# Optimization experiments

Measured on AMD Instinct MI355X. Metric: run time of the kernel, lower is better.

## Reference

```python
import jax, jax.numpy as jnp
import numpy as np

B, GH, GW, DIM, NH = 1, 48, 64, 1536, 16
HD = DIM // NH          # 96
C = HD // 2             # 48, divisible by 3 as the rope split requires
L = max(GH, GW)


def setup_inputs() -> dict:
    key = jax.random.key(0)
    ks = jax.random.split(key, 6)
    x = jax.random.normal(ks[0], (B, GH * GW, DIM), jnp.float32)
    w_init = lambda k: jax.random.normal(k, (DIM, DIM), jnp.float32) * 0.02
    # rope frequency table: theta[p, j] = p / 10000^(j/C); freqs = exp(i*theta)
    pos = jnp.arange(L, dtype=jnp.float32)[:, None]
    inv = 10000.0 ** (-jnp.arange(C, dtype=jnp.float32) / C)
    theta = pos * inv[None, :]
    return {
        "x": x,
        "wq": w_init(ks[1]), "bq": jnp.zeros((DIM,), jnp.float32),
        "wk": w_init(ks[2]), "bk": jnp.zeros((DIM,), jnp.float32),
        "wv": w_init(ks[3]), "bv": jnp.zeros((DIM,), jnp.float32),
        "wo": w_init(ks[4]), "bo": jnp.zeros((DIM,), jnp.float32),
        "freqs_cos": jnp.cos(theta), "freqs_sin": jnp.sin(theta),
        "h": GH, "w": GW,
    }


def rope_apply_spatial(x, freqs_cos, freqs_sin, h, w):
    # x: [b, s, n, d] with s == h*w. Complex rotation done in real arithmetic.
    b, s, n, d = x.shape
    c = d // 2
    c3 = c // 3
    # channel groups: [0:c3] identity (ones), [c3:2c3] rotated by h-position,
    # [2c3:3c3] rotated by w-position  (matches freqs.split + cat in torch)
    cos_hw = jnp.concatenate([
        jnp.ones((h, w, c3), x.dtype),
        jnp.broadcast_to(freqs_cos[:h, None, c3:2 * c3], (h, w, c3)),
        jnp.broadcast_to(freqs_cos[None, :w, 2 * c3:3 * c3], (h, w, c3)),
    ], axis=-1).reshape(1, s, 1, c)
    sin_hw = jnp.concatenate([
        jnp.zeros((h, w, c3), x.dtype),
        jnp.broadcast_to(freqs_sin[:h, None, c3:2 * c3], (h, w, c3)),
        jnp.broadcast_to(freqs_sin[None, :w, 2 * c3:3 * c3], (h, w, c3)),
    ], axis=-1).reshape(1, s, 1, c)
    xc = x.reshape(b, s, n, c, 2)
    xr, xi = xc[..., 0], xc[..., 1]
    yr = xr * cos_hw - xi * sin_hw
    yi = xr * sin_hw + xi * cos_hw
    return jnp.stack([yr, yi], axis=-1).reshape(b, s, n, d)


def reference(x, wq, bq, wk, bk, wv, bv, wo, bo, freqs_cos, freqs_sin, h, w):
    b, s, _ = x.shape
    q = (x @ wq + bq).reshape(b, s, NH, HD)
    k = (x @ wk + bk).reshape(b, s, NH, HD)
    v = (x @ wv + bv).reshape(b, s, NH, HD)
    q = rope_apply_spatial(q, freqs_cos, freqs_sin, h, w)
    k = rope_apply_spatial(k, freqs_cos, freqs_sin, h, w)
    scale = 1.0 / jnp.sqrt(jnp.asarray(HD, q.dtype))
    scores = jnp.einsum('bqnd,bknd->bnqk', q, k) * scale  # [b, n, s, s]
    attn = jax.nn.softmax(scores, axis=-1)
    out = jnp.einsum('bnqk,bknd->bqnd', attn, v).reshape(b, s, NH * HD)
    return out @ wo + bo
```

## Files before the change

### kernel.cpp

```cpp
#include <hip/hip_runtime.h>
#include <math.h>

#define S_LEN 3072
#define DIM 1536
#define NHEADS 16
#define HDIM 96
#define NPAIR 48

typedef __attribute__((ext_vector_type(8))) _Float16 half8;
typedef __attribute__((ext_vector_type(4))) _Float16 half4v;
typedef __attribute__((ext_vector_type(2))) _Float16 half2v;
typedef __attribute__((ext_vector_type(4))) float f32x4;

__device__ inline void gload16(const void* g, void* l) {
    __builtin_amdgcn_global_load_lds(
        (const __attribute__((address_space(1))) void*)g,
        (__attribute__((address_space(3))) void*)l, 16, 0, 0);
}

__device__ inline unsigned int packh2(float a, float b) {
    _Float16 ha = (_Float16)a, hb = (_Float16)b;
    unsigned short ua = *(unsigned short*)&ha;
    unsigned short ub = *(unsigned short*)&hb;
    return (unsigned int)ua | ((unsigned int)ub << 16);
}

__global__ __launch_bounds__(256)
void convert_f32_f16(const float* __restrict__ src, _Float16* __restrict__ dst, int n4)
{
    int i = blockIdx.x * 256 + threadIdx.x;
    if (i < n4) {
        float4 v = *(const float4*)&src[(size_t)i * 4];
        half4v h = { (_Float16)v.x, (_Float16)v.y, (_Float16)v.z, (_Float16)v.w };
        *(half4v*)&dst[(size_t)i * 4] = h;
    }
}

__global__ __launch_bounds__(256)
void transpose_w(const float* __restrict__ w0, const float* __restrict__ w1,
                 const float* __restrict__ w2, const float* __restrict__ w3,
                 _Float16* __restrict__ wt)
{
    __shared__ _Float16 t[64][68];
    const int z = blockIdx.z;
    const float* W = (z == 0) ? w0 : (z == 1) ? w1 : (z == 2) ? w2 : w3;
    _Float16* O = wt + (size_t)z * DIM * DIM;
    const int k0 = blockIdx.y * 64, n0 = blockIdx.x * 64;
    const int tid = threadIdx.x;
    const int r = tid >> 4, c4 = (tid & 15) * 4;
#pragma unroll
    for (int g = 0; g < 4; g++) {
        int kk = r + g * 16;
        float4 v = *(const float4*)&W[(size_t)(k0 + kk) * DIM + n0 + c4];
        t[c4 + 0][kk] = (_Float16)v.x; t[c4 + 1][kk] = (_Float16)v.y;
        t[c4 + 2][kk] = (_Float16)v.z; t[c4 + 3][kk] = (_Float16)v.w;
    }
    __syncthreads();
    const int nr = tid >> 2, ks = (tid & 3) * 16;
#pragma unroll
    for (int s = 0; s < 4; s++)
        *(ushort4*)&O[(size_t)(n0 + nr) * DIM + k0 + ks + s * 4] =
            *(ushort4*)&t[nr][ks + s * 4];
}

template<bool QKV>
__global__ __launch_bounds__(256)
void gemm_f16(const _Float16* __restrict__ X,
              const _Float16* __restrict__ W0t, const _Float16* __restrict__ W1t,
              const _Float16* __restrict__ W2t,
              const float* __restrict__ B0, const float* __restrict__ B1,
              const float* __restrict__ B2,
              const float* __restrict__ fc, const float* __restrict__ fs,
              void* __restrict__ outv)
{
    __shared__ __align__(16) _Float16 As[128][64];
    __shared__ __align__(16) _Float16 Bs[128][64];

    const int tid = threadIdx.x;
    const int w = tid >> 6, lane = tid & 63;
    const int ln = lane & 15, quad = lane >> 4;
    const int bz = blockIdx.z;
    const _Float16* Wt = W0t; const float* bias = B0;
    if (QKV) { if (bz == 1) { Wt = W1t; bias = B1; } else if (bz == 2) { Wt = W2t; bias = B2; } }
    const int m0 = blockIdx.y * 128, n0 = blockIdx.x * 128;
    const int wm = w >> 1, wn = w & 1;
    const int row8 = lane >> 3, cch = lane & 7;
    const int gch = cch ^ row8;

    f32x4 acc[4][4];
#pragma unroll
    for (int i = 0; i < 4; i++)
#pragma unroll
        for (int j = 0; j < 4; j++) acc[i][j] = (f32x4){0.f, 0.f, 0.f, 0.f};

    for (int k0 = 0; k0 < DIM; k0 += 64) {
        __syncthreads();
#pragma unroll
        for (int j = 0; j < 4; j++) {
            const int r = w * 32 + j * 8;
            gload16(X  + (size_t)(m0 + r + row8) * DIM + k0 + gch * 8, &As[r][0]);
            gload16(Wt + (size_t)(n0 + r + row8) * DIM + k0 + gch * 8, &Bs[r][0]);
        }
        __syncthreads();

        half8 a[4][2], b[4][2];
#pragma unroll
        for (int mt = 0; mt < 4; mt++) {
            int m = wm * 64 + mt * 16 + ln;
#pragma unroll
            for (int ks = 0; ks < 2; ks++) {
                int s = (ks * 4 + quad) ^ (ln & 7);
                a[mt][ks] = *(const half8*)&As[m][s * 8];
            }
        }
#pragma unroll
        for (int nt = 0; nt < 4; nt++) {
            int n = wn * 64 + nt * 16 + ln;
#pragma unroll
            for (int ks = 0; ks < 2; ks++) {
                int s = (ks * 4 + quad) ^ (ln & 7);
                b[nt][ks] = *(const half8*)&Bs[n][s * 8];
            }
        }
#pragma unroll
        for (int ks = 0; ks < 2; ks++)
#pragma unroll
            for (int mt = 0; mt < 4; mt++)
#pragma unroll
                for (int nt = 0; nt < 4; nt++)
                    acc[mt][nt] = __builtin_amdgcn_mfma_f32_16x16x32_f16(
                        a[mt][ks], b[nt][ks], acc[mt][nt], 0, 0, 0);
    }

#pragma unroll
    for (int nt = 0; nt < 4; nt++) {
        int col = n0 + wn * 64 + nt * 16 + ln;
        float bv = bias[col];
        int head = col / HDIM, hd = col % HDIM;
        int jc = hd >> 1;
        bool isreal = (ln & 1) == 0;
#pragma unroll
        for (int mt = 0; mt < 4; mt++) {
            int row0 = m0 + wm * 64 + mt * 16 + quad * 4;
            if (QKV && bz == 2) {
                half4v p;
#pragma unroll
                for (int r = 0; r < 4; r++) p[r] = (_Float16)(acc[mt][nt][r] + bv);
                *(half4v*)&((_Float16*)outv)[(((size_t)2 * NHEADS + head) * HDIM + hd) * S_LEN + row0] = p;
            } else if (QKV) {
                float v[4], vp[4];
#pragma unroll
                for (int r = 0; r < 4; r++) v[r] = acc[mt][nt][r] + bv;
#pragma unroll
                for (int r = 0; r < 4; r++) vp[r] = __shfl_xor(v[r], 1);
#pragma unroll
                for (int r = 0; r < 4; r++) {
                    int srow = row0 + r;
                    int pos = (jc < 32) ? (srow >> 6) : (srow & 63);
                    float c  = fc[pos * NPAIR + jc];
                    float sn = fs[pos * NPAIR + jc];
                    float xr = isreal ? v[r] : vp[r];
                    float xi = isreal ? vp[r] : v[r];
                    float rot = isreal ? (xr * c - xi * sn) : (xr * sn + xi * c);
                    float outval = (jc < 16) ? v[r] : rot;
                    ((_Float16*)outv)[(((size_t)bz * NHEADS + head) * S_LEN + srow) * HDIM + hd]
                        = (_Float16)outval;
                }
            } else {
#pragma unroll
                for (int r = 0; r < 4; r++)
                    ((float*)outv)[(size_t)(row0 + r) * DIM + col] = acc[mt][nt][r] + bv;
            }
        }
    }
}

__global__ __launch_bounds__(128, 2)
void attn_mfma_kernel(const _Float16* __restrict__ qh, const _Float16* __restrict__ kh,
                      const _Float16* __restrict__ vtg, _Float16* __restrict__ aoh)
{
    __shared__ __align__(16) _Float16 Ks[64][104];
    __shared__ __align__(16) _Float16 Vt[96][64];
    __shared__ __align__(16) _Float16 Pl[4][16][72];

    const int tid  = threadIdx.x;
    const int wid  = tid >> 6;
    const int lane = tid & 63;
    const int ln   = lane & 15;
    const int quad = lane >> 4;
    const int h    = blockIdx.y;
    const int q0   = blockIdx.x * 64;
    const float scale_ = 0.10206207261596577f;
    const int NT = S_LEN / 64;

    half8 aq[2][3];
#pragma unroll
    for (int qs = 0; qs < 2; qs++) {
        const _Float16* qrow = qh + (((size_t)h * S_LEN) + q0 + (wid * 2 + qs) * 16 + ln) * HDIM;
#pragma unroll
        for (int kb3 = 0; kb3 < 3; kb3++) {
            half8 a = *(const half8*)&qrow[kb3 * 32 + quad * 8];
            half8 v;
#pragma unroll
            for (int i = 0; i < 8; i++) v[i] = (_Float16)((float)a[i] * scale_);
            aq[qs][kb3] = v;
        }
    }

    f32x4 o[2][6];
#pragma unroll
    for (int qs = 0; qs < 2; qs++)
#pragma unroll
        for (int dn = 0; dn < 6; dn++) o[qs][dn] = (f32x4){0.f, 0.f, 0.f, 0.f};
    float m_[2] = {-INFINITY, -INFINITY}, l_[2] = {0.f, 0.f};

    const _Float16* kbase = kh + ((size_t)h * S_LEN) * HDIM;
    const _Float16* vbase = vtg + ((size_t)h * HDIM) * S_LEN;

    const int krow = tid >> 1, kc0 = (tid & 1) * 6;
    const _Float16* ksrc0 = kbase + (size_t)krow * HDIM + kc0 * 8;
    _Float16* kdst = &Ks[krow][kc0 * 8];
    const int vd0 = tid >> 3, vc = tid & 7;
    const _Float16* vsrc0 = vbase + (size_t)vd0 * S_LEN + vc * 8;
    _Float16* vdst = &Vt[vd0][(vc ^ (vd0 & 7)) * 8];

    uint4 kp0, kp1, kp2, kp3, kp4, kp5, vp0, vp1, vp2, vp3, vp4, vp5;
    kp0 = *(const uint4*)(ksrc0 + 0 * 8);  kp1 = *(const uint4*)(ksrc0 + 1 * 8);
    kp2 = *(const uint4*)(ksrc0 + 2 * 8);  kp3 = *(const uint4*)(ksrc0 + 3 * 8);
    kp4 = *(const uint4*)(ksrc0 + 4 * 8);  kp5 = *(const uint4*)(ksrc0 + 5 * 8);
    vp0 = *(const uint4*)(vsrc0 + 0 * 16 * S_LEN);
    vp1 = *(const uint4*)(vsrc0 + 1 * 16 * S_LEN);
    vp2 = *(const uint4*)(vsrc0 + 2 * 16 * S_LEN);
    vp3 = *(const uint4*)(vsrc0 + 3 * 16 * S_LEN);
    vp4 = *(const uint4*)(vsrc0 + 4 * 16 * S_LEN);
    vp5 = *(const uint4*)(vsrc0 + 5 * 16 * S_LEN);

    for (int kt = 0; kt < NT; ++kt) {
        __syncthreads();
        *(uint4*)(kdst + 0 * 8) = kp0;  *(uint4*)(kdst + 1 * 8) = kp1;
        *(uint4*)(kdst + 2 * 8) = kp2;  *(uint4*)(kdst + 3 * 8) = kp3;
        *(uint4*)(kdst + 4 * 8) = kp4;  *(uint4*)(kdst + 5 * 8) = kp5;
        *(uint4*)(vdst + 0 * 16 * 64) = vp0;  *(uint4*)(vdst + 1 * 16 * 64) = vp1;
        *(uint4*)(vdst + 2 * 16 * 64) = vp2;  *(uint4*)(vdst + 3 * 16 * 64) = vp3;
        *(uint4*)(vdst + 4 * 16 * 64) = vp4;  *(uint4*)(vdst + 5 * 16 * 64) = vp5;
        __syncthreads();

        if (kt + 1 < NT) {
            const _Float16* ks2 = ksrc0 + (size_t)(kt + 1) * 64 * HDIM;
            const _Float16* vs2 = vsrc0 + (kt + 1) * 64;
            kp0 = *(const uint4*)(ks2 + 0 * 8);  kp1 = *(const uint4*)(ks2 + 1 * 8);
            kp2 = *(const uint4*)(ks2 + 2 * 8);  kp3 = *(const uint4*)(ks2 + 3 * 8);
            kp4 = *(const uint4*)(ks2 + 4 * 8);  kp5 = *(const uint4*)(ks2 + 5 * 8);
            vp0 = *(const uint4*)(vs2 + 0 * 16 * S_LEN);
            vp1 = *(const uint4*)(vs2 + 1 * 16 * S_LEN);
            vp2 = *(const uint4*)(vs2 + 2 * 16 * S_LEN);
            vp3 = *(const uint4*)(vs2 + 3 * 16 * S_LEN);
            vp4 = *(const uint4*)(vs2 + 4 * 16 * S_LEN);
            vp5 = *(const uint4*)(vs2 + 5 * 16 * S_LEN);
        }

        f32x4 s[2][4];
#pragma unroll
        for (int nb = 0; nb < 4; nb++) {
            half8 ak0 = *(const half8*)&Ks[nb * 16 + ln][0 * 32 + quad * 8];
            half8 ak1 = *(const half8*)&Ks[nb * 16 + ln][1 * 32 + quad * 8];
            half8 ak2 = *(const half8*)&Ks[nb * 16 + ln][2 * 32 + quad * 8];
#pragma unroll
            for (int qs = 0; qs < 2; qs++) {
                f32x4 acc = (f32x4){0.f, 0.f, 0.f, 0.f};
                acc = __builtin_amdgcn_mfma_f32_16x16x32_f16(ak0, aq[qs][0], acc, 0, 0, 0);
                acc = __builtin_amdgcn_mfma_f32_16x16x32_f16(ak1, aq[qs][1], acc, 0, 0, 0);
                acc = __builtin_amdgcn_mfma_f32_16x16x32_f16(ak2, aq[qs][2], acc, 0, 0, 0);
                s[qs][nb] = acc;
            }
        }

        float al[2];
#pragma unroll
        for (int qs = 0; qs < 2; qs++) {
            float mx = s[qs][0][0];
#pragma unroll
            for (int nb = 0; nb < 4; nb++)
#pragma unroll
                for (int r = 0; r < 4; r++) mx = fmaxf(mx, s[qs][nb][r]);
            mx = fmaxf(mx, __shfl_xor(mx, 16));
            mx = fmaxf(mx, __shfl_xor(mx, 32));
            float mn = fmaxf(m_[qs], mx);
            al[qs] = __expf(m_[qs] - mn);
            m_[qs] = mn;
            float rs = 0.f;
#pragma unroll
            for (int nb = 0; nb < 4; nb++)
#pragma unroll
                for (int r = 0; r < 4; r++) {
                    float p = __expf(s[qs][nb][r] - mn);
                    s[qs][nb][r] = p;
                    rs += p;
                }
            rs += __shfl_xor(rs, 16);
            rs += __shfl_xor(rs, 32);
            l_[qs] = l_[qs] * al[qs] + rs;

#pragma unroll
            for (int nb = 0; nb < 4; nb++) {
                uint2 u;
                u.x = packh2(s[qs][nb][0], s[qs][nb][1]);
                u.y = packh2(s[qs][nb][2], s[qs][nb][3]);
                *(uint2*)&Pl[wid * 2 + qs][ln][nb * 16 + quad * 4] = u;
            }
#pragma unroll
            for (int dn = 0; dn < 6; dn++)
#pragma unroll
                for (int r = 0; r < 4; r++) o[qs][dn][r] *= al[qs];
        }

        half8 ap[2][2];
#pragma unroll
        for (int qs = 0; qs < 2; qs++)
#pragma unroll
            for (int c = 0; c < 2; c++)
                ap[qs][c] = *(const half8*)&Pl[wid * 2 + qs][ln][c * 32 + quad * 8];
#pragma unroll
        for (int c = 0; c < 2; c++) {
#pragma unroll
            for (int dn = 0; dn < 6; dn++) {
                int row = dn * 16 + ln;
                int slot = (c * 4 + quad) ^ (ln & 7);
                half8 av = *(const half8*)&Vt[row][slot * 8];
                o[0][dn] = __builtin_amdgcn_mfma_f32_16x16x32_f16(av, ap[0][c], o[0][dn], 0, 0, 0);
                o[1][dn] = __builtin_amdgcn_mfma_f32_16x16x32_f16(av, ap[1][c], o[1][dn], 0, 0, 0);
            }
        }
    }

#pragma unroll
    for (int qs = 0; qs < 2; qs++) {
        const float invl = 1.f / l_[qs];
        const size_t rowbase = (size_t)(q0 + (wid * 2 + qs) * 16 + ln) * DIM + h * HDIM;
#pragma unroll
        for (int dn = 0; dn < 6; dn++) {
            half4v p;
#pragma unroll
            for (int r = 0; r < 4; r++) p[r] = (_Float16)(o[qs][dn][r] * invl);
            *(half4v*)&aoh[rowbase + dn * 16 + quad * 4] = p;
        }
    }
}

extern "C" void kernel_launch(void* const* d_in, const int* in_sizes, int n_in,
                              void* d_out, int out_size, void* d_ws, size_t ws_size,
                              hipStream_t stream) {
    const float* x  = (const float*)d_in[0];
    const float* wq = (const float*)d_in[1];
    const float* bq = (const float*)d_in[2];
    const float* wk = (const float*)d_in[3];
    const float* bk = (const float*)d_in[4];
    const float* wv = (const float*)d_in[5];
    const float* bv = (const float*)d_in[6];
    const float* wo = (const float*)d_in[7];
    const float* bo = (const float*)d_in[8];
    const float* fc = (const float*)d_in[9];
    const float* fs = (const float*)d_in[10];
    float* out = (float*)d_out;

    const size_t per  = (size_t)NHEADS * S_LEN * HDIM;
    const size_t dim2 = (size_t)DIM * DIM;
    _Float16* hws  = (_Float16*)d_ws;
    _Float16* qkvh = hws;
    _Float16* qh   = qkvh;
    _Float16* kh   = qkvh + per;
    _Float16* vth  = qkvh + 2 * per;
    _Float16* xh   = hws + 3 * per;
    _Float16* wth  = hws + 4 * per;

    convert_f32_f16<<<(int)((S_LEN * DIM / 4 + 255) / 256), 256, 0, stream>>>(
        x, xh, S_LEN * DIM / 4);
    transpose_w<<<dim3(DIM / 64, DIM / 64, 4), 256, 0, stream>>>(wq, wk, wv, wo, wth);

    gemm_f16<true><<<dim3(DIM / 128, S_LEN / 128, 3), 256, 0, stream>>>(
        xh, wth, wth + dim2, wth + 2 * dim2, bq, bk, bv, fc, fs, qkvh);
    attn_mfma_kernel<<<dim3(S_LEN / 64, NHEADS), 128, 0, stream>>>(qh, kh, vth, xh);
    gemm_f16<false><<<dim3(DIM / 128, S_LEN / 128, 1), 256, 0, stream>>>(
        xh, wth + 3 * dim2, nullptr, nullptr, bo, nullptr, nullptr, fc, fs, out);
}
```

Measured before the change: 334.9 us.

## Split attention KV range across two wave pairs and drop P LDS round-trip

The attention kernel now launches 256 threads per block. Two wave-pairs each process half of the key/value sequence, and their partial softmax states are merged through LDS at the end. P is kept in registers and fed to 16x16x16 MFMAs with a padded, swizzled V tile, so the Pl shared-memory buffer goes away. Softmax uses exp2 with log2e folded into the Q scale, and rescaling is skipped unless a row max grows by more than a threshold. The V prefetch is moved after the softmax, with sched barriers. This aims to raise occupancy and parallelism and cut LDS traffic, at the cost of a final merge step, more LDS per block and register pressure under launch_bounds(256,3).

```diff
diff --git a/kernel.cpp b/kernel.cpp
--- a/kernel.cpp
+++ b/kernel.cpp
@@ -16,13 +16,6 @@
     __builtin_amdgcn_global_load_lds(
         (const __attribute__((address_space(1))) void*)g,
         (__attribute__((address_space(3))) void*)l, 16, 0, 0);
-}
-
-__device__ inline unsigned int packh2(float a, float b) {
-    _Float16 ha = (_Float16)a, hb = (_Float16)b;
-    unsigned short ua = *(unsigned short*)&ha;
-    unsigned short ub = *(unsigned short*)&hb;
-    return (unsigned int)ua | ((unsigned int)ub << 16);
 }
 
 __global__ __launch_bounds__(256)
@@ -175,35 +168,36 @@
     }
 }
 
-__global__ __launch_bounds__(128, 2)
+__global__ __launch_bounds__(256, 3)
 void attn_mfma_kernel(const _Float16* __restrict__ qh, const _Float16* __restrict__ kh,
                       const _Float16* __restrict__ vtg, _Float16* __restrict__ aoh)
 {
-    __shared__ __align__(16) _Float16 Ks[64][104];
-    __shared__ __align__(16) _Float16 Vt[96][64];
-    __shared__ __align__(16) _Float16 Pl[4][16][72];
+    __shared__ __align__(16) _Float16 Ks[2][64][104];
+    __shared__ __align__(16) _Float16 Vt[2][96][72];
 
     const int tid  = threadIdx.x;
     const int wid  = tid >> 6;
+    const int p    = wid >> 1;
+    const int wp   = wid & 1;
     const int lane = tid & 63;
     const int ln   = lane & 15;
     const int quad = lane >> 4;
     const int h    = blockIdx.y;
     const int q0   = blockIdx.x * 64;
-    const float scale_ = 0.10206207261596577f;
-    const int NT = S_LEN / 64;
+    const float scale_ = 0.10206207261596577f * 1.4426950408889634f;
+    const int NT = (S_LEN / 2) / 64;
 
     half8 aq[2][3];
 #pragma unroll
     for (int qs = 0; qs < 2; qs++) {
-        const _Float16* qrow = qh + (((size_t)h * S_LEN) + q0 + (wid * 2 + qs) * 16 + ln) * HDIM;
-#pragma unroll
-        for (int kb3 = 0; kb3 < 3; kb3++) {
-            half8 a = *(const half8*)&qrow[kb3 * 32 + quad * 8];
+        const _Float16* qrow = qh + (((size_t)h * S_LEN) + q0 + (wp * 2 + qs) * 16 + ln) * HDIM;
+#pragma unroll
+        for (int kb = 0; kb < 3; kb++) {
+            half8 a = *(const half8*)&qrow[kb * 32 + quad * 8];
             half8 v;
 #pragma unroll
             for (int i = 0; i < 8; i++) v[i] = (_Float16)((float)a[i] * scale_);
-            aq[qs][kb3] = v;
+            aq[qs][kb] = v;
         }
     }
 
@@ -214,15 +208,16 @@
         for (int dn = 0; dn < 6; dn++) o[qs][dn] = (f32x4){0.f, 0.f, 0.f, 0.f};
     float m_[2] = {-INFINITY, -INFINITY}, l_[2] = {0.f, 0.f};
 
-    const _Float16* kbase = kh + ((size_t)h * S_LEN) * HDIM;
-    const _Float16* vbase = vtg + ((size_t)h * HDIM) * S_LEN;
-
-    const int krow = tid >> 1, kc0 = (tid & 1) * 6;
+    const _Float16* kbase = kh + ((size_t)h * S_LEN + p * (S_LEN / 2)) * HDIM;
+    const _Float16* vbase = vtg + (size_t)h * HDIM * S_LEN + p * (S_LEN / 2);
+
+    const int tp = tid & 127;
+    const int krow = tp >> 1, kc0 = (tp & 1) * 6;
     const _Float16* ksrc0 = kbase + (size_t)krow * HDIM + kc0 * 8;
-    _Float16* kdst = &Ks[krow][kc0 * 8];
-    const int vd0 = tid >> 3, vc = tid & 7;
+    _Float16* kdst = &Ks[p][krow][kc0 * 8];
+    const int vd0 = tp >> 3, vc = tp & 7;
     const _Float16* vsrc0 = vbase + (size_t)vd0 * S_LEN + vc * 8;
-    _Float16* vdst = &Vt[vd0][(vc ^ (vd0 & 7)) * 8];
+    _Float16* vdst = &Vt[p][vd0][(vc ^ (vd0 & 7)) * 8];
 
     uint4 kp0, kp1, kp2, kp3, kp4, kp5, vp0, vp1, vp2, vp3, vp4, vp5;
     kp0 = *(const uint4*)(ksrc0 + 0 * 8);  kp1 = *(const uint4*)(ksrc0 + 1 * 8);
@@ -240,109 +235,134 @@
         *(uint4*)(kdst + 0 * 8) = kp0;  *(uint4*)(kdst + 1 * 8) = kp1;
         *(uint4*)(kdst + 2 * 8) = kp2;  *(uint4*)(kdst + 3 * 8) = kp3;
         *(uint4*)(kdst + 4 * 8) = kp4;  *(uint4*)(kdst + 5 * 8) = kp5;
-        *(uint4*)(vdst + 0 * 16 * 64) = vp0;  *(uint4*)(vdst + 1 * 16 * 64) = vp1;
-        *(uint4*)(vdst + 2 * 16 * 64) = vp2;  *(uint4*)(vdst + 3 * 16 * 64) = vp3;
-        *(uint4*)(vdst + 4 * 16 * 64) = vp4;  *(uint4*)(vdst + 5 * 16 * 64) = vp5;
+        *(uint4*)(vdst + 0 * 16 * 72) = vp0;  *(uint4*)(vdst + 1 * 16 * 72) = vp1;
+        *(uint4*)(vdst + 2 * 16 * 72) = vp2;  *(uint4*)(vdst + 3 * 16 * 72) = vp3;
+        *(uint4*)(vdst + 4 * 16 * 72) = vp4;  *(uint4*)(vdst + 5 * 16 * 72) = vp5;
         __syncthreads();
 
         if (kt + 1 < NT) {
             const _Float16* ks2 = ksrc0 + (size_t)(kt + 1) * 64 * HDIM;
-            const _Float16* vs2 = vsrc0 + (kt + 1) * 64;
             kp0 = *(const uint4*)(ks2 + 0 * 8);  kp1 = *(const uint4*)(ks2 + 1 * 8);
             kp2 = *(const uint4*)(ks2 + 2 * 8);  kp3 = *(const uint4*)(ks2 + 3 * 8);
             kp4 = *(const uint4*)(ks2 + 4 * 8);  kp5 = *(const uint4*)(ks2 + 5 * 8);
+            __builtin_amdgcn_sched_barrier(0);
+        }
+
+        f32x4 s[2][4];
+#pragma unroll
+        for (int nb = 0; nb < 4; nb++) {
+            half8 ak0 = *(const half8*)&Ks[p][nb * 16 + ln][0 * 32 + quad * 8];
+            half8 ak1 = *(const half8*)&Ks[p][nb * 16 + ln][1 * 32 + quad * 8];
+            half8 ak2 = *(const half8*)&Ks[p][nb * 16 + ln][2 * 32 + quad * 8];
+#pragma unroll
+            for (int qs = 0; qs < 2; qs++) {
+                f32x4 acc = (f32x4){0.f, 0.f, 0.f, 0.f};
+                acc = __builtin_amdgcn_mfma_f32_16x16x32_f16(ak0, aq[qs][0], acc, 0, 0, 0);
+                acc = __builtin_amdgcn_mfma_f32_16x16x32_f16(ak1, aq[qs][1], acc, 0, 0, 0);
+                acc = __builtin_amdgcn_mfma_f32_16x16x32_f16(ak2, aq[qs][2], acc, 0, 0, 0);
+                s[qs][nb] = acc;
+            }
+        }
+
+        half4v ap[2][4];
+#pragma unroll
+        for (int qs = 0; qs < 2; qs++) {
+            float ma = fmaxf(fmaxf(s[qs][0][0], s[qs][0][1]), fmaxf(s[qs][0][2], s[qs][0][3]));
+            float mb = fmaxf(fmaxf(s[qs][1][0], s[qs][1][1]), fmaxf(s[qs][1][2], s[qs][1][3]));
+            float mc = fmaxf(fmaxf(s[qs][2][0], s[qs][2][1]), fmaxf(s[qs][2][2], s[qs][2][3]));
+            float md = fmaxf(fmaxf(s[qs][3][0], s[qs][3][1]), fmaxf(s[qs][3][2], s[qs][3][3]));
+            float mx = fmaxf(fmaxf(ma, mb), fmaxf(mc, md));
+            if (!__all(mx <= m_[qs] + 8.0f)) {
+                mx = fmaxf(mx, __shfl_xor(mx, 16));
+                mx = fmaxf(mx, __shfl_xor(mx, 32));
+                float mn = fmaxf(m_[qs], mx);
+                float al = __builtin_amdgcn_exp2f(m_[qs] - mn);
+                m_[qs] = mn;
+                l_[qs] *= al;
+#pragma unroll
+                for (int dn = 0; dn < 6; dn++)
+#pragma unroll
+                    for (int r = 0; r < 4; r++) o[qs][dn][r] *= al;
+            }
+            float rs = 0.f;
+            float mq = m_[qs];
+#pragma unroll
+            for (int nb = 0; nb < 4; nb++) {
+                float p0 = __builtin_amdgcn_exp2f(s[qs][nb][0] - mq);
+                float p1 = __builtin_amdgcn_exp2f(s[qs][nb][1] - mq);
+                float p2 = __builtin_amdgcn_exp2f(s[qs][nb][2] - mq);
+                float p3 = __builtin_amdgcn_exp2f(s[qs][nb][3] - mq);
+                rs += (p0 + p1) + (p2 + p3);
+                half4v pk = { (_Float16)p0, (_Float16)p1, (_Float16)p2, (_Float16)p3 };
+                ap[qs][nb] = pk;
+            }
+            l_[qs] += rs;
+        }
+
+        if (kt + 1 < NT) {
+            const _Float16* vs2 = vsrc0 + (kt + 1) * 64;
             vp0 = *(const uint4*)(vs2 + 0 * 16 * S_LEN);
             vp1 = *(const uint4*)(vs2 + 1 * 16 * S_LEN);
             vp2 = *(const uint4*)(vs2 + 2 * 16 * S_LEN);
             vp3 = *(const uint4*)(vs2 + 3 * 16 * S_LEN);
             vp4 = *(const uint4*)(vs2 + 4 * 16 * S_LEN);
             vp5 = *(const uint4*)(vs2 + 5 * 16 * S_LEN);
-        }
-
-        f32x4 s[2][4];
+            __builtin_amdgcn_sched_barrier(0);
+        }
+
 #pragma unroll
         for (int nb = 0; nb < 4; nb++) {
-            half8 ak0 = *(const half8*)&Ks[nb * 16 + ln][0 * 32 + quad * 8];
-            half8 ak1 = *(const half8*)&Ks[nb * 16 + ln][1 * 32 + quad * 8];
-            half8 ak2 = *(const half8*)&Ks[nb * 16 + ln][2 * 32 + quad * 8];
-#pragma unroll
-            for (int qs = 0; qs < 2; qs++) {
-                f32x4 acc = (f32x4){0.f, 0.f, 0.f, 0.f};
-                acc = __builtin_amdgcn_mfma_f32_16x16x32_f16(ak0, aq[qs][0], acc, 0, 0, 0);
-                acc = __builtin_amdgcn_mfma_f32_16x16x32_f16(ak1, aq[qs][1], acc, 0, 0, 0);
-                acc = __builtin_amdgcn_mfma_f32_16x16x32_f16(ak2, aq[qs][2], acc, 0, 0, 0);
-                s[qs][nb] = acc;
-            }
-        }
-
-        float al[2];
+            const int off = (((nb * 2 + (quad >> 1)) ^ (ln & 7)) * 8) + (quad & 1) * 4;
+#pragma unroll
+            for (int dn = 0; dn < 6; dn++) {
+                half4v av = *(const half4v*)&Vt[p][dn * 16 + ln][off];
+                o[0][dn] = __builtin_amdgcn_mfma_f32_16x16x16f16(av, ap[0][nb], o[0][dn], 0, 0, 0);
+                o[1][dn] = __builtin_amdgcn_mfma_f32_16x16x16f16(av, ap[1][nb], o[1][dn], 0, 0, 0);
+            }
+        }
+    }
+
+    __syncthreads();
+    float lt[2];
+#pragma unroll
+    for (int qs = 0; qs < 2; qs++) {
+        float l = l_[qs];
+        l += __shfl_xor(l, 16);
+        l += __shfl_xor(l, 32);
+        lt[qs] = l;
+    }
+    float*  scr = (float*)&Ks[0][0][0];
+    float2* mlb = (float2*)&Vt[0][0][0];
+    if (p == 1) {
 #pragma unroll
         for (int qs = 0; qs < 2; qs++) {
-            float mx = s[qs][0][0];
-#pragma unroll
-            for (int nb = 0; nb < 4; nb++)
-#pragma unroll
-                for (int r = 0; r < 4; r++) mx = fmaxf(mx, s[qs][nb][r]);
-            mx = fmaxf(mx, __shfl_xor(mx, 16));
-            mx = fmaxf(mx, __shfl_xor(mx, 32));
-            float mn = fmaxf(m_[qs], mx);
-            al[qs] = __expf(m_[qs] - mn);
-            m_[qs] = mn;
-            float rs = 0.f;
-#pragma unroll
-            for (int nb = 0; nb < 4; nb++)
-#pragma unroll
-                for (int r = 0; r < 4; r++) {
-                    float p = __expf(s[qs][nb][r] - mn);
-                    s[qs][nb][r] = p;
-                    rs += p;
-                }
-            rs += __shfl_xor(rs, 16);
-            rs += __shfl_xor(rs, 32);
-            l_[qs] = l_[qs] * al[qs] + rs;
-
-#pragma unroll
-            for (int nb = 0; nb < 4; nb++) {
-                uint2 u;
-                u.x = packh2(s[qs][nb][0], s[qs][nb][1]);
-                u.y = packh2(s[qs][nb][2], s[qs][nb][3]);
-                *(uint2*)&Pl[wid * 2 + qs][ln][nb * 16 + quad * 4] = u;
-            }
+            int row = (wp * 2 + qs) * 16 + ln;
+            if (quad == 0) mlb[row] = make_float2(m_[qs], lt[qs]);
 #pragma unroll
             for (int dn = 0; dn < 6; dn++)
-#pragma unroll
-                for (int r = 0; r < 4; r++) o[qs][dn][r] *= al[qs];
-        }
-
-        half8 ap[2][2];
-#pragma unroll
-        for (int qs = 0; qs < 2; qs++)
-#pragma unroll
-            for (int c = 0; c < 2; c++)
-                ap[qs][c] = *(const half8*)&Pl[wid * 2 + qs][ln][c * 32 + quad * 8];
-#pragma unroll
-        for (int c = 0; c < 2; c++) {
+                *(f32x4*)&scr[row * 100 + dn * 16 + quad * 4] = o[qs][dn];
+        }
+    }
+    __syncthreads();
+    if (p == 0) {
+#pragma unroll
+        for (int qs = 0; qs < 2; qs++) {
+            int row = (wp * 2 + qs) * 16 + ln;
+            float2 ml1 = mlb[row];
+            float mm = fmaxf(m_[qs], ml1.x);
+            float a0 = __builtin_amdgcn_exp2f(m_[qs] - mm);
+            float a1 = __builtin_amdgcn_exp2f(ml1.x - mm);
+            float li = 1.0f / (lt[qs] * a0 + ml1.y * a1);
+            const size_t rowbase = (size_t)(q0 + row) * DIM + h * HDIM;
 #pragma unroll
             for (int dn = 0; dn < 6; dn++) {
-                int row = dn * 16 + ln;
-                int slot = (c * 4 + quad) ^ (ln & 7);
-                half8 av = *(const half8*)&Vt[row][slot * 8];
-                o[0][dn] = __builtin_amdgcn_mfma_f32_16x16x32_f16(av, ap[0][c], o[0][dn], 0, 0, 0);
-                o[1][dn] = __builtin_amdgcn_mfma_f32_16x16x32_f16(av, ap[1][c], o[1][dn], 0, 0, 0);
-            }
-        }
-    }
-
-#pragma unroll
-    for (int qs = 0; qs < 2; qs++) {
-        const float invl = 1.f / l_[qs];
-        const size_t rowbase = (size_t)(q0 + (wid * 2 + qs) * 16 + ln) * DIM + h * HDIM;
-#pragma unroll
-        for (int dn = 0; dn < 6; dn++) {
-            half4v p;
-#pragma unroll
-            for (int r = 0; r < 4; r++) p[r] = (_Float16)(o[qs][dn][r] * invl);
-            *(half4v*)&aoh[rowbase + dn * 16 + quad * 4] = p;
+                f32x4 o1 = *(const f32x4*)&scr[row * 100 + dn * 16 + quad * 4];
+                half4v pk;
+#pragma unroll
+                for (int r = 0; r < 4; r++)
+                    pk[r] = (_Float16)((o[qs][dn][r] * a0 + o1[r] * a1) * li);
+                *(half4v*)&aoh[rowbase + dn * 16 + quad * 4] = pk;
+            }
         }
     }
 }
@@ -379,7 +399,7 @@
 
     gemm_f16<true><<<dim3(DIM / 128, S_LEN / 128, 3), 256, 0, stream>>>(
         xh, wth, wth + dim2, wth + 2 * dim2, bq, bk, bv, fc, fs, qkvh);
-    attn_mfma_kernel<<<dim3(S_LEN / 64, NHEADS), 128, 0, stream>>>(qh, kh, vth, xh);
+    attn_mfma_kernel<<<dim3(S_LEN / 64, NHEADS), 256, 0, stream>>>(qh, kh, vth, xh);
     gemm_f16<false><<<dim3(DIM / 128, S_LEN / 128, 1), 256, 0, stream>>>(
         xh, wth + 3 * dim2, nullptr, nullptr, bo, nullptr, nullptr, fc, fs, out);
 }
```

Result: no change. 331.1 us (-1.1%).
